# Kernel optimization log

Hardware: AMD Instinct MI355X
Metric: run time of the kernel (lower is better)

Reference implementation:

```python
import jax, jax.numpy as jnp
import numpy as np

EPS = 1e-8  # torch cosine_similarity default eps


def setup_inputs() -> dict:
    key = jax.random.key(0)
    k1, k2, k3 = jax.random.split(key, 3)
    bsz, sent_len, cont_dim, mp_dim = 16, 512, 768, 20
    repres = jax.random.normal(k1, (bsz, sent_len, cont_dim), dtype=jnp.float32)
    max_att = jax.random.normal(k2, (bsz, sent_len, cont_dim), dtype=jnp.float32)
    # nn.Parameter initialized uniform_(-1, 1)
    weight = jax.random.uniform(k3, (mp_dim, cont_dim), dtype=jnp.float32, minval=-1.0, maxval=1.0)
    return {"repres": repres, "max_att": max_att, "weight": weight}


def reference(repres, max_att, weight):
    # Original math: a = repres[:,None,:] * w[None], b = max_att[:,None,:] * w[None]
    # cos = <a,b> / (max(||a||,eps) * max(||b||,eps)) along last dim.
    # Fused form: never materialize [N, mp_dim, cont_dim]; contract with w^2 directly.
    bsz, sent_len, cont_dim = repres.shape
    r = repres.reshape(-1, cont_dim)   # [N, D]
    m = max_att.reshape(-1, cont_dim)  # [N, D]
    w2 = weight * weight               # [P, D]
    dot = jnp.einsum('nd,pd->np', r * m, w2)              # [N, P]
    n1 = jnp.sqrt(jnp.einsum('nd,pd->np', r * r, w2))     # [N, P]
    n2 = jnp.sqrt(jnp.einsum('nd,pd->np', m * m, w2))     # [N, P]
    cos = dot / (jnp.maximum(n1, EPS) * jnp.maximum(n2, EPS))
    return cos.reshape(bsz, sent_len, weight.shape[0])
```

## Files before the change

### kernel.cpp

```cpp
#include <hip/hip_runtime.h>
#include <math.h>
#include <stdint.h>


static constexpr int D_DIM   = 768;
static constexpr int NP      = 20;
static constexpr int NROWS   = 8192;
static constexpr int ROWS_PB = 16;
static constexpr int BLOCKS  = NROWS / ROWS_PB;
static constexpr int NTHR    = 256;
static constexpr int KW      = 192;
static constexpr int KSLICE  = 32;
static constexpr int NSLICES = KW / KSLICE;

typedef short  short8  __attribute__((ext_vector_type(8)));
typedef float  float4v __attribute__((ext_vector_type(4)));

static constexpr int B_CSTR = 776 * 2;
static constexpr int LDS_SZ = NP * B_CSTR;

__device__ __forceinline__ unsigned short bf16_rne(float x) {
  unsigned u = __float_as_uint(x);
  u += 0x7FFFu + ((u >> 16) & 1u);
  return (unsigned short)(u >> 16);
}
__device__ __forceinline__ float bf16f(unsigned short h) {
  return __uint_as_float(((unsigned)h) << 16);
}

__global__ __launch_bounds__(NTHR) void atte_cos_v3(
    const float* __restrict__ repres,
    const float* __restrict__ max_att,
    const float* __restrict__ weight,
    float* __restrict__ out)
{
  const int tid  = threadIdx.x;
  const int wave = tid >> 6;
  const int lane = tid & 63;
  const int row0 = blockIdx.x * ROWS_PB;
  const int k0   = wave * KW;
  const int part = lane >> 4;
  const int mrow = lane & 15;

  __shared__ __align__(16) char smem[31104];

  const float* ar = repres  + (size_t)(row0 + mrow) * D_DIM + k0 + part * 8;
  const float* am = max_att + (size_t)(row0 + mrow) * D_DIM + k0 + part * 8;

  float4 fr[2][2], fm[2][2];
  fr[0][0] = *(const float4*)(ar + 0 * KSLICE);
  fr[0][1] = *(const float4*)(ar + 0 * KSLICE + 4);
  fm[0][0] = *(const float4*)(am + 0 * KSLICE);
  fm[0][1] = *(const float4*)(am + 0 * KSLICE + 4);
  fr[1][0] = *(const float4*)(ar + 1 * KSLICE);
  fr[1][1] = *(const float4*)(ar + 1 * KSLICE + 4);
  fm[1][0] = *(const float4*)(am + 1 * KSLICE);
  fm[1][1] = *(const float4*)(am + 1 * KSLICE + 4);

  {
    const float4* wsrc = (const float4*)weight;
#pragma unroll
    for (int it = 0; it < 15; ++it) {
      const int i   = it * NTHR + tid;
      const int col = i / 192;
      const int kq  = i - col * 192;
      float4 w = wsrc[i];
      ushort4 h;
      h.x = bf16_rne(w.x * w.x);
      h.y = bf16_rne(w.y * w.y);
      h.z = bf16_rne(w.z * w.z);
      h.w = bf16_rne(w.w * w.w);
      *(ushort4*)(smem + col * B_CSTR + kq * 8) = h;
    }
  }

  __syncthreads();

  const char* b0p = smem + (lane & 15) * B_CSTR + (k0 + part * 8) * 2;
  const int   c1c = min(16 + (lane & 15), NP - 1);
  const char* b1p = smem + c1c * B_CSTR + (k0 + part * 8) * 2;

  float4v acc[6] = {};

#pragma unroll
  for (int s = 0; s < NSLICES; ++s) {
    float rv[8], mv[8];
    *(float4*)&rv[0] = fr[s & 1][0];
    *(float4*)&rv[4] = fr[s & 1][1];
    *(float4*)&mv[0] = fm[s & 1][0];
    *(float4*)&mv[4] = fm[s & 1][1];

    if (s + 2 < NSLICES) {
      fr[s & 1][0] = *(const float4*)(ar + (s + 2) * KSLICE);
      fr[s & 1][1] = *(const float4*)(ar + (s + 2) * KSLICE + 4);
      fm[s & 1][0] = *(const float4*)(am + (s + 2) * KSLICE);
      fm[s & 1][1] = *(const float4*)(am + (s + 2) * KSLICE + 4);
    }

    short8 a0h, a0l, a1h, a2h;
#pragma unroll
    for (int j = 0; j < 8; ++j) {
      const float pm = rv[j] * mv[j];
      const float pr = rv[j] * rv[j];
      const float pq = mv[j] * mv[j];
      const unsigned short h = bf16_rne(pm);
      a0h[j] = (short)h;
      a0l[j] = (short)bf16_rne(pm - bf16f(h));
      a1h[j] = (short)bf16_rne(pr);
      a2h[j] = (short)bf16_rne(pq);
    }

    const short8 b0 = *(const short8*)(b0p + s * 64);
    const short8 b1 = *(const short8*)(b1p + s * 64);

    acc[0] = __builtin_amdgcn_mfma_f32_16x16x32_bf16(a0h, b0, acc[0], 0, 0, 0);
    acc[0] = __builtin_amdgcn_mfma_f32_16x16x32_bf16(a0l, b0, acc[0], 0, 0, 0);
    acc[1] = __builtin_amdgcn_mfma_f32_16x16x32_bf16(a0h, b1, acc[1], 0, 0, 0);
    acc[1] = __builtin_amdgcn_mfma_f32_16x16x32_bf16(a0l, b1, acc[1], 0, 0, 0);
    acc[2] = __builtin_amdgcn_mfma_f32_16x16x32_bf16(a1h, b0, acc[2], 0, 0, 0);
    acc[3] = __builtin_amdgcn_mfma_f32_16x16x32_bf16(a1h, b1, acc[3], 0, 0, 0);
    acc[4] = __builtin_amdgcn_mfma_f32_16x16x32_bf16(a2h, b0, acc[4], 0, 0, 0);
    acc[5] = __builtin_amdgcn_mfma_f32_16x16x32_bf16(a2h, b1, acc[5], 0, 0, 0);
  }

  __syncthreads();
#pragma unroll
  for (int qc = 0; qc < 6; ++qc)
    *(float4v*)(smem + ((qc * 4 + wave) * 64 + lane) * 16) = acc[qc];
  __syncthreads();

  if (wave < 2) {
    const int ct = wave;
    float4v c0 = {}, c1 = {}, c2 = {};
#pragma unroll
    for (int wv = 0; wv < 4; ++wv) {
      c0 += *(const float4v*)(smem + (((0 * 2 + ct) * 4 + wv) * 64 + lane) * 16);
      c1 += *(const float4v*)(smem + (((1 * 2 + ct) * 4 + wv) * 64 + lane) * 16);
      c2 += *(const float4v*)(smem + (((2 * 2 + ct) * 4 + wv) * 64 + lane) * 16);
    }
    const int col = ct * 16 + (lane & 15);
    if (col < NP) {
      const int rbase = row0 + (lane >> 4) * 4;
#pragma unroll
      for (int r = 0; r < 4; ++r) {
        const float n1 = fmaxf(sqrtf(c1[r]), 1e-8f);
        const float n2 = fmaxf(sqrtf(c2[r]), 1e-8f);
        out[(size_t)(rbase + r) * NP + col] = c0[r] / (n1 * n2);
      }
    }
  }
}

extern "C" void kernel_launch(void* const* d_in, const int* in_sizes, int n_in,
                              void* d_out, int out_size, void* d_ws, size_t ws_size,
                              hipStream_t stream) {
  atte_cos_v3<<<BLOCKS, NTHR, 0, stream>>>(
      (const float*)d_in[0], (const float*)d_in[1],
      (const float*)d_in[2], (float*)d_out);
}
```

Baseline: 90.72 us.

## Load squared weights directly into registers and split K across eight waves

Drops the cooperative staging of squared bf16 weights in LDS and the barrier that followed it. Each lane now loads its own weight fragments from global memory and squares and converts them in registers. Blocks grow to 512 threads so K is split across 8 waves, and all activation slices are loaded up front instead of through a two-deep prefetch. This shrinks LDS use, which should raise occupancy and shorten the per-block prologue, at the cost of more register pressure and redundant weight reads, which rely on L2 hits.

```diff
diff --git a/kernel.cpp b/kernel.cpp
--- a/kernel.cpp
+++ b/kernel.cpp
@@ -8,16 +8,14 @@
 static constexpr int NROWS   = 8192;
 static constexpr int ROWS_PB = 16;
 static constexpr int BLOCKS  = NROWS / ROWS_PB;
-static constexpr int NTHR    = 256;
-static constexpr int KW      = 192;
+static constexpr int NTHR    = 512;
+static constexpr int NW      = 8;
+static constexpr int KW      = D_DIM / NW;
 static constexpr int KSLICE  = 32;
 static constexpr int NSLICES = KW / KSLICE;
 
 typedef short  short8  __attribute__((ext_vector_type(8)));
 typedef float  float4v __attribute__((ext_vector_type(4)));
-
-static constexpr int B_CSTR = 776 * 2;
-static constexpr int LDS_SZ = NP * B_CSTR;
 
 __device__ __forceinline__ unsigned short bf16_rne(float x) {
   unsigned u = __float_as_uint(x);
@@ -28,7 +26,7 @@
   return __uint_as_float(((unsigned)h) << 16);
 }
 
-__global__ __launch_bounds__(NTHR) void atte_cos_v3(
+__global__ __launch_bounds__(NTHR, 4) void atte_cos_v4(
     const float* __restrict__ repres,
     const float* __restrict__ max_att,
     const float* __restrict__ weight,
@@ -42,60 +40,55 @@
   const int part = lane >> 4;
   const int mrow = lane & 15;
 
-  __shared__ __align__(16) char smem[31104];
+  __shared__ __align__(16) char smem[6 * NW * 64 * 16];
 
   const float* ar = repres  + (size_t)(row0 + mrow) * D_DIM + k0 + part * 8;
   const float* am = max_att + (size_t)(row0 + mrow) * D_DIM + k0 + part * 8;
 
-  float4 fr[2][2], fm[2][2];
-  fr[0][0] = *(const float4*)(ar + 0 * KSLICE);
-  fr[0][1] = *(const float4*)(ar + 0 * KSLICE + 4);
-  fm[0][0] = *(const float4*)(am + 0 * KSLICE);
-  fm[0][1] = *(const float4*)(am + 0 * KSLICE + 4);
-  fr[1][0] = *(const float4*)(ar + 1 * KSLICE);
-  fr[1][1] = *(const float4*)(ar + 1 * KSLICE + 4);
-  fm[1][0] = *(const float4*)(am + 1 * KSLICE);
-  fm[1][1] = *(const float4*)(am + 1 * KSLICE + 4);
+  const int cA = lane & 15;
+  const int cB = min(16 + (lane & 15), NP - 1);
+  const float* wA = weight + (size_t)cA * D_DIM + k0 + part * 8;
+  const float* wB = weight + (size_t)cB * D_DIM + k0 + part * 8;
 
-  {
-    const float4* wsrc = (const float4*)weight;
+  float4 fr[NSLICES][2], fm[NSLICES][2];
 #pragma unroll
-    for (int it = 0; it < 15; ++it) {
-      const int i   = it * NTHR + tid;
-      const int col = i / 192;
-      const int kq  = i - col * 192;
-      float4 w = wsrc[i];
-      ushort4 h;
-      h.x = bf16_rne(w.x * w.x);
-      h.y = bf16_rne(w.y * w.y);
-      h.z = bf16_rne(w.z * w.z);
-      h.w = bf16_rne(w.w * w.w);
-      *(ushort4*)(smem + col * B_CSTR + kq * 8) = h;
+  for (int s = 0; s < NSLICES; ++s) {
+    fr[s][0] = *(const float4*)(ar + s * KSLICE);
+    fr[s][1] = *(const float4*)(ar + s * KSLICE + 4);
+    fm[s][0] = *(const float4*)(am + s * KSLICE);
+    fm[s][1] = *(const float4*)(am + s * KSLICE + 4);
+  }
+  float4 fwA[NSLICES][2], fwB[NSLICES][2];
+#pragma unroll
+  for (int s = 0; s < NSLICES; ++s) {
+    fwA[s][0] = *(const float4*)(wA + s * KSLICE);
+    fwA[s][1] = *(const float4*)(wA + s * KSLICE + 4);
+    fwB[s][0] = *(const float4*)(wB + s * KSLICE);
+    fwB[s][1] = *(const float4*)(wB + s * KSLICE + 4);
+  }
+
+  short8 bh0[NSLICES], bh1[NSLICES];
+#pragma unroll
+  for (int s = 0; s < NSLICES; ++s) {
+    float wa[8], wb[8];
+    *(float4*)&wa[0] = fwA[s][0]; *(float4*)&wa[4] = fwA[s][1];
+    *(float4*)&wb[0] = fwB[s][0]; *(float4*)&wb[4] = fwB[s][1];
+#pragma unroll
+    for (int j = 0; j < 8; ++j) {
+      bh0[s][j] = (short)bf16_rne(wa[j] * wa[j]);
+      bh1[s][j] = (short)bf16_rne(wb[j] * wb[j]);
     }
   }
-
-  __syncthreads();
-
-  const char* b0p = smem + (lane & 15) * B_CSTR + (k0 + part * 8) * 2;
-  const int   c1c = min(16 + (lane & 15), NP - 1);
-  const char* b1p = smem + c1c * B_CSTR + (k0 + part * 8) * 2;
 
   float4v acc[6] = {};
 
 #pragma unroll
   for (int s = 0; s < NSLICES; ++s) {
     float rv[8], mv[8];
-    *(float4*)&rv[0] = fr[s & 1][0];
-    *(float4*)&rv[4] = fr[s & 1][1];
-    *(float4*)&mv[0] = fm[s & 1][0];
-    *(float4*)&mv[4] = fm[s & 1][1];
-
-    if (s + 2 < NSLICES) {
-      fr[s & 1][0] = *(const float4*)(ar + (s + 2) * KSLICE);
-      fr[s & 1][1] = *(const float4*)(ar + (s + 2) * KSLICE + 4);
-      fm[s & 1][0] = *(const float4*)(am + (s + 2) * KSLICE);
-      fm[s & 1][1] = *(const float4*)(am + (s + 2) * KSLICE + 4);
-    }
+    *(float4*)&rv[0] = fr[s][0];
+    *(float4*)&rv[4] = fr[s][1];
+    *(float4*)&mv[0] = fm[s][0];
+    *(float4*)&mv[4] = fm[s][1];
 
     short8 a0h, a0l, a1h, a2h;
 #pragma unroll
@@ -110,8 +103,8 @@
       a2h[j] = (short)bf16_rne(pq);
     }
 
-    const short8 b0 = *(const short8*)(b0p + s * 64);
-    const short8 b1 = *(const short8*)(b1p + s * 64);
+    const short8 b0 = bh0[s];
+    const short8 b1 = bh1[s];
 
     acc[0] = __builtin_amdgcn_mfma_f32_16x16x32_bf16(a0h, b0, acc[0], 0, 0, 0);
     acc[0] = __builtin_amdgcn_mfma_f32_16x16x32_bf16(a0l, b0, acc[0], 0, 0, 0);
@@ -123,20 +116,19 @@
     acc[5] = __builtin_amdgcn_mfma_f32_16x16x32_bf16(a2h, b1, acc[5], 0, 0, 0);
   }
 
-  __syncthreads();
 #pragma unroll
   for (int qc = 0; qc < 6; ++qc)
-    *(float4v*)(smem + ((qc * 4 + wave) * 64 + lane) * 16) = acc[qc];
+    *(float4v*)(smem + ((qc * NW + wave) * 64 + lane) * 16) = acc[qc];
   __syncthreads();
 
   if (wave < 2) {
     const int ct = wave;
     float4v c0 = {}, c1 = {}, c2 = {};
 #pragma unroll
-    for (int wv = 0; wv < 4; ++wv) {
-      c0 += *(const float4v*)(smem + (((0 * 2 + ct) * 4 + wv) * 64 + lane) * 16);
-      c1 += *(const float4v*)(smem + (((1 * 2 + ct) * 4 + wv) * 64 + lane) * 16);
-      c2 += *(const float4v*)(smem + (((2 * 2 + ct) * 4 + wv) * 64 + lane) * 16);
+    for (int wv = 0; wv < NW; ++wv) {
+      c0 += *(const float4v*)(smem + (((0 * 2 + ct) * NW + wv) * 64 + lane) * 16);
+      c1 += *(const float4v*)(smem + (((1 * 2 + ct) * NW + wv) * 64 + lane) * 16);
+      c2 += *(const float4v*)(smem + (((2 * 2 + ct) * NW + wv) * 64 + lane) * 16);
     }
     const int col = ct * 16 + (lane & 15);
     if (col < NP) {
@@ -154,7 +146,7 @@
 extern "C" void kernel_launch(void* const* d_in, const int* in_sizes, int n_in,
                               void* d_out, int out_size, void* d_ws, size_t ws_size,
                               hipStream_t stream) {
-  atte_cos_v3<<<BLOCKS, NTHR, 0, stream>>>(
+  atte_cos_v4<<<BLOCKS, NTHR, 0, stream>>>(
       (const float*)d_in[0], (const float*)d_in[1],
       (const float*)d_in[2], (float*)d_out);
 }
```

Result: no change. 90.82 us (+0.1%).
